# Performance work log

Measured on AMD Instinct MI355X. Metric: run time of the kernel, lower is better.

The kernel has to match this reference:

```python
import jax, jax.numpy as jnp
from jax import lax
import numpy as np

IN, HID, OUT = 28, 64, 10


def _lstm_layer(x_seq, W_ih, W_hh, b_ih, b_hh):
    # x_seq: [B, T, in]; PyTorch gate order: i, f, g, o (stacked along 4H)
    B = x_seq.shape[0]
    H = W_hh.shape[1]
    # Precompute input projection for all timesteps: [B, T, 4H]
    x_proj = jnp.einsum('bti,gi->btg', x_seq, W_ih) + b_ih + b_hh

    def step(carry, xt):
        h, c = carry
        gates = xt + h @ W_hh.T  # [B, 4H]
        i, f, g, o = jnp.split(gates, 4, axis=-1)
        i = jax.nn.sigmoid(i)
        f = jax.nn.sigmoid(f)
        g = jnp.tanh(g)
        o = jax.nn.sigmoid(o)
        c = f * c + i * g
        h = o * jnp.tanh(c)
        return (h, c), h

    h0 = jnp.zeros((B, H), x_seq.dtype)
    (_, _), hs = lax.scan(step, (h0, h0), jnp.swapaxes(x_proj, 0, 1))
    return jnp.swapaxes(hs, 0, 1)  # [B, T, H]


def setup_inputs() -> dict:
    key = jax.random.key(0)
    ks = jax.random.split(key, 12)
    s_in = 1.0 / np.sqrt(HID)
    u = lambda k, shape: jax.random.uniform(k, shape, jnp.float32, -s_in, s_in)
    return {
        'x': jax.random.normal(ks[0], (16384, 1, 28, 28), jnp.float32),
        'W_ih0': u(ks[1], (4 * HID, IN)),
        'W_hh0': u(ks[2], (4 * HID, HID)),
        'b_ih0': u(ks[3], (4 * HID,)),
        'b_hh0': u(ks[4], (4 * HID,)),
        'W_ih1': u(ks[5], (4 * HID, HID)),
        'W_hh1': u(ks[6], (4 * HID, HID)),
        'b_ih1': u(ks[7], (4 * HID,)),
        'b_hh1': u(ks[8], (4 * HID,)),
        'W_lin': u(ks[9], (OUT, HID)),
        'b_lin': u(ks[10], (OUT,)),
    }


def reference(x, W_ih0, W_hh0, b_ih0, b_hh0, W_ih1, W_hh1, b_ih1, b_hh1, W_lin, b_lin):
    # (N, C, H, W) -> (N, C*H, W): sequence of rows, feature = W = 28
    x = x.reshape(x.shape[0], -1, x.shape[-1])
    h1 = _lstm_layer(x, W_ih0, W_hh0, b_ih0, b_hh0)   # [B, T, 64]
    h2 = _lstm_layer(h1, W_ih1, W_hh1, b_ih1, b_hh1)  # [B, T, 64]
    last = h2[:, -1, :]
    return last @ W_lin.T + b_lin  # [B, 10]
```

## Files before the change

### kernel.cpp

```cpp
#include <hip/hip_runtime.h>


typedef _Float16 half8 __attribute__((ext_vector_type(8)));
typedef float floatx4 __attribute__((ext_vector_type(4)));

#define NFRAG 112
#define WS_BIAS_OFF (NFRAG * 1024)
#define K2 2.8853900817779268f

#if __has_builtin(__builtin_amdgcn_exp2f)
#define EXP2(v) __builtin_amdgcn_exp2f(v)
#else
#define EXP2(v) __expf(0.6931471805599453f * (v))
#endif
#define RCP(v) __builtin_amdgcn_rcpf(v)

__global__ void prep_kernel(const float* __restrict__ Wih0, const float* __restrict__ Whh0,
                            const float* __restrict__ bih0, const float* __restrict__ bhh0,
                            const float* __restrict__ Wih1, const float* __restrict__ Whh1,
                            const float* __restrict__ bih1, const float* __restrict__ bhh1,
                            _Float16* __restrict__ wA, float* __restrict__ wBias) {
    int idx = blockIdx.x * blockDim.x + threadIdx.x;
    if (idx < NFRAG * 512) {
        int f = idx >> 9, slot = idx & 511;
        int lane = slot >> 3, j = slot & 7;
        int mt, kt, layer;
        if (f < 48) { layer = 0; mt = f / 3; kt = f % 3; }
        else        { layer = 1; int f2 = f - 48; mt = f2 >> 2; kt = f2 & 3; }
        int m = mt * 16 + (lane & 15);
        int k = kt * 32 + (lane >> 4) * 8 + j;
        int u = m >> 2, g = m & 3;
        int row = g * 64 + u;
        float v;
        if (layer == 0) {
            if (k < 28)       v = Wih0[row * 28 + k];
            else if (k == 28) v = bih0[row] + bhh0[row];
            else if (k < 32)  v = 0.f;
            else              v = Whh0[row * 64 + (k - 32)];
        } else {
            if (k < 64)       v = Wih1[row * 64 + k];
            else              v = Whh1[row * 64 + (k - 64)];
        }
        float s = (g == 2) ? K2 : -1.4426950408889634f;
        wA[idx] = (_Float16)(v * s);
    } else if (idx < NFRAG * 512 + 256) {
        int m = idx - NFRAG * 512;
        int g = m & 3;
        int row = g * 64 + (m >> 2);
        float s = (g == 2) ? K2 : -1.4426950408889634f;
        wBias[m] = (bih1[row] + bhh1[row]) * s;
    }
}

template <int N>
__device__ __forceinline__ void gate_batch(const floatx4* acc, float* c,
                                           _Float16* const* planes, const int* offs) {
    float ei[N], ef[N], eg[N], eo[N];
    #pragma unroll
    for (int i = 0; i < N; ++i) {
        floatx4 a = acc[i];
        ei[i] = EXP2(a[0]);
        ef[i] = EXP2(a[1]);
        eg[i] = EXP2(a[2]);
        eo[i] = EXP2(a[3]);
    }
    float num[N], rd[N], po[N];
    #pragma unroll
    for (int i = 0; i < N; ++i) {
        float pi = 1.0f + ei[i];
        float pf = 1.0f + ef[i];
        float pg = 1.0f + eg[i];
        po[i] = 1.0f + eo[i];
        float m = pg * pi;
        num[i] = c[i] * m + (eg[i] - 1.0f) * pf;
        rd[i]  = RCP(pf * m);
    }
    float ec[N];
    #pragma unroll
    for (int i = 0; i < N; ++i) {
        float cn = num[i] * rd[i];
        c[i] = cn;
        ec[i] = EXP2(K2 * cn);
    }
    #pragma unroll
    for (int i = 0; i < N; ++i) {
        float r2 = RCP(ec[i] * po[i] + po[i]);
        planes[i][offs[i]] = (_Float16)((ec[i] - 1.0f) * r2);
    }
}

__launch_bounds__(512, 4)
__global__ void lstm_mfma(const float* __restrict__ x,
                          const _Float16* __restrict__ wA,
                          const float* __restrict__ wBias,
                          const float* __restrict__ Wlin, const float* __restrict__ blin,
                          float* __restrict__ out) {
    __shared__ __align__(16) _Float16 h0p[2][2048];
    __shared__ __align__(16) _Float16 h1p[2][2048];
    __shared__ __align__(16) _Float16 xb[2][1024];
    __shared__ float wlin_s[640];
    __shared__ float blin_s[10];

    const int lane = threadIdx.x;
    const int w    = threadIdx.y;
    const int tid  = w * 64 + lane;
    const int quad = lane >> 4;
    const int col  = lane & 15;
    const int l8   = lane * 8;
    const int nord = (w >> 2) & 1;

    half8 A0[2][3], A1[2][4];
    floatx4 bias1[2];
    int hwr0[2];
    #pragma unroll
    for (int j = 0; j < 2; ++j) {
        const int MT = 2 * w + j;
        #pragma unroll
        for (int kt = 0; kt < 3; ++kt)
            A0[j][kt] = *(const half8*)(wA + (MT * 3 + kt) * 512 + l8);
        #pragma unroll
        for (int kt = 0; kt < 4; ++kt)
            A1[j][kt] = *(const half8*)(wA + (48 + MT * 4 + kt) * 512 + l8);
        const int u = MT * 4 + quad;
        bias1[j] = *(const floatx4*)(wBias + u * 4);
        hwr0[j] = (u >> 5) * 512 + (((u >> 3) & 3) * 16 + col) * 8 + (u & 7);
    }

    const int ks = tid & 31;
    const bool xvalid = ks < 28;
    const int xbi = tid >> 5;
    const float* xg = x + (blockIdx.x * 32 + xbi) * 784 + ks;
    const int xstg = ((ks >> 3) * 16 + xbi) * 8 + (ks & 7);

    {
        ((int*)&h0p[1][0])[tid * 2 + 0] = 0;
        ((int*)&h0p[1][0])[tid * 2 + 1] = 0;
        ((int*)&h1p[1][0])[tid * 2 + 0] = 0;
        ((int*)&h1p[1][0])[tid * 2 + 1] = 0;
        float xv0 = xvalid ? xg[0] : 0.f;
        float xv1 = xvalid ? xg[16 * 784] : 0.f;
        _Float16 cpad = (ks == 28) ? (_Float16)1.0f : (_Float16)0.0f;
        xb[0][xstg]       = xvalid ? (_Float16)xv0 : cpad;
        xb[0][xstg + 512] = xvalid ? (_Float16)xv1 : cpad;
        xb[1][xstg]       = cpad;
        xb[1][xstg + 512] = cpad;
    }
    __syncthreads();

    float c0[2][2] = {{0.f, 0.f}, {0.f, 0.f}};
    float c1[2][2] = {{0.f, 0.f}, {0.f, 0.f}};

    for (int p = -1; p <= 27; ++p) {
        const int pr  = p & 1;
        const int pr1 = pr ^ 1;
        const bool doL0 = (p < 27);
        const bool doL1 = (p >= 0);

        float xn0 = 0.f, xn1 = 0.f;
        if (p <= 25 && xvalid) {
            xn0 = xg[(p + 2) * 28];
            xn1 = xg[16 * 784 + (p + 2) * 28];
        }

        #pragma unroll
        for (int pass = 0; pass < 2; ++pass) {
            const int in = nord ^ pass;
            const int hb = in << 10;

            half8 bx, bh0[2];
            if (doL0) bx = *(const half8*)&xb[pr1][(in << 9) + l8];
            #pragma unroll
            for (int kt = 0; kt < 2; ++kt)
                bh0[kt] = *(const half8*)&h0p[pr][hb + kt * 512 + l8];

            floatx4 acc0[2], acc1[2];
            if (doL0) {
                #pragma unroll
                for (int j = 0; j < 2; ++j) {
                    acc0[j] = __builtin_amdgcn_mfma_f32_16x16x32_f16(
                                  A0[j][0], bx, (floatx4){0.f, 0.f, 0.f, 0.f}, 0, 0, 0);
                    #pragma unroll
                    for (int kt = 0; kt < 2; ++kt)
                        acc0[j] = __builtin_amdgcn_mfma_f32_16x16x32_f16(
                                      A0[j][kt + 1], bh0[kt], acc0[j], 0, 0, 0);
                }
            }
            if (doL1) {
                #pragma unroll
                for (int j = 0; j < 2; ++j) {
                    acc1[j] = bias1[j];
                    #pragma unroll
                    for (int kt = 0; kt < 2; ++kt)
                        acc1[j] = __builtin_amdgcn_mfma_f32_16x16x32_f16(
                                      A1[j][kt], bh0[kt], acc1[j], 0, 0, 0);
                }
                half8 bh1[2];
                #pragma unroll
                for (int kt = 0; kt < 2; ++kt)
                    bh1[kt] = *(const half8*)&h1p[pr1][hb + kt * 512 + l8];
                #pragma unroll
                for (int j = 0; j < 2; ++j)
                    #pragma unroll
                    for (int kt = 0; kt < 2; ++kt)
                        acc1[j] = __builtin_amdgcn_mfma_f32_16x16x32_f16(
                                      A1[j][kt + 2], bh1[kt], acc1[j], 0, 0, 0);
            }

            const int offA = hwr0[0] + hb;
            const int offB = hwr0[1] + hb;
            if (doL0 && doL1) {
                floatx4 a4[4] = {acc0[0], acc0[1], acc1[0], acc1[1]};
                float   cc[4] = {c0[pass][0], c0[pass][1], c1[pass][0], c1[pass][1]};
                _Float16* pl[4] = {h0p[pr1], h0p[pr1], h1p[pr], h1p[pr]};
                int offs[4] = {offA, offB, offA, offB};
                gate_batch<4>(a4, cc, pl, offs);
                c0[pass][0] = cc[0]; c0[pass][1] = cc[1];
                c1[pass][0] = cc[2]; c1[pass][1] = cc[3];
            } else if (doL0) {
                floatx4 a2[2] = {acc0[0], acc0[1]};
                _Float16* pl[2] = {h0p[pr1], h0p[pr1]};
                int offs[2] = {offA, offB};
                gate_batch<2>(a2, c0[pass], pl, offs);
            } else {
                floatx4 a2[2] = {acc1[0], acc1[1]};
                _Float16* pl[2] = {h1p[pr], h1p[pr]};
                int offs[2] = {offA, offB};
                gate_batch<2>(a2, c1[pass], pl, offs);
            }
        }

        if (p <= 25 && xvalid) {
            xb[pr][xstg]       = (_Float16)xn0;
            xb[pr][xstg + 512] = (_Float16)xn1;
        }
        __syncthreads();
    }

    wlin_s[tid] = Wlin[tid];
    if (tid < 128) wlin_s[512 + tid] = Wlin[512 + tid];
    if (tid < 10)  blin_s[tid] = blin[tid];
    __syncthreads();
    if (tid < 320) {
        int b = tid / 10, o = tid - b * 10;
        float a = blin_s[o];
        #pragma unroll 8
        for (int uu = 0; uu < 64; ++uu) {
            float hv = (float)h1p[1][((b >> 4) * 2 + (uu >> 5)) * 512 + (((uu >> 3) & 3) * 16 + (b & 15)) * 8 + (uu & 7)];
            a += wlin_s[o * 64 + uu] * hv;
        }
        out[(blockIdx.x * 32 + b) * 10 + o] = a;
    }
}

extern "C" void kernel_launch(void* const* d_in, const int* in_sizes, int n_in,
                              void* d_out, int out_size, void* d_ws, size_t ws_size,
                              hipStream_t stream) {
    const float* x    = (const float*)d_in[0];
    const float* Wih0 = (const float*)d_in[1];
    const float* Whh0 = (const float*)d_in[2];
    const float* bih0 = (const float*)d_in[3];
    const float* bhh0 = (const float*)d_in[4];
    const float* Wih1 = (const float*)d_in[5];
    const float* Whh1 = (const float*)d_in[6];
    const float* bih1 = (const float*)d_in[7];
    const float* bhh1 = (const float*)d_in[8];
    const float* Wlin = (const float*)d_in[9];
    const float* blin = (const float*)d_in[10];
    float* out = (float*)d_out;

    _Float16* wA    = (_Float16*)d_ws;
    float*    wBias = (float*)((char*)d_ws + WS_BIAS_OFF);

    prep_kernel<<<225, 256, 0, stream>>>(Wih0, Whh0, bih0, bhh0,
                                         Wih1, Whh1, bih1, bhh1, wA, wBias);
    lstm_mfma<<<512, dim3(64, 8), 0, stream>>>(x, wA, wBias, Wlin, blin, out);
}
```

Measured before the change: 172.8 us.

## Merge two batch passes per step and peel loop into specialized phases

Each phase now processes both 16-column batch halves in one pass, issuing all MFMAs together and calling gate_batch on 8 accumulators at once, which exposes more independent MFMA and transcendental work per wavefront. The timestep loop is peeled into compile-time specialised phases, unrolled by two, so parity and layer-enable predicates become constants. Input staging switches to float2 loads of two adjacent elements per thread. The cost is higher register pressure from doubled live accumulators under the 512x4 launch bound, which could cause spills.

```diff
diff --git a/kernel.cpp b/kernel.cpp
--- a/kernel.cpp
+++ b/kernel.cpp
@@ -1,7 +1,8 @@
 #include <hip/hip_runtime.h>
 
 
-typedef _Float16 half8 __attribute__((ext_vector_type(8)));
+typedef _Float16 half8  __attribute__((ext_vector_type(8)));
+typedef _Float16 half2v __attribute__((ext_vector_type(2)));
 typedef float floatx4 __attribute__((ext_vector_type(4)));
 
 #define NFRAG 112
@@ -107,11 +108,10 @@
     const int quad = lane >> 4;
     const int col  = lane & 15;
     const int l8   = lane * 8;
-    const int nord = (w >> 2) & 1;
 
     half8 A0[2][3], A1[2][4];
     floatx4 bias1[2];
-    int hwr0[2];
+    int woff[2][2];
     #pragma unroll
     for (int j = 0; j < 2; ++j) {
         const int MT = 2 * w + j;
@@ -123,118 +123,147 @@
             A1[j][kt] = *(const half8*)(wA + (48 + MT * 4 + kt) * 512 + l8);
         const int u = MT * 4 + quad;
         bias1[j] = *(const floatx4*)(wBias + u * 4);
-        hwr0[j] = (u >> 5) * 512 + (((u >> 3) & 3) * 16 + col) * 8 + (u & 7);
-    }
-
-    const int ks = tid & 31;
-    const bool xvalid = ks < 28;
-    const int xbi = tid >> 5;
-    const float* xg = x + (blockIdx.x * 32 + xbi) * 784 + ks;
-    const int xstg = ((ks >> 3) * 16 + xbi) * 8 + (ks & 7);
+        const int hwr0 = (u >> 5) * 512 + (((u >> 3) & 3) * 16 + col) * 8 + (u & 7);
+        woff[j][0] = hwr0;
+        woff[j][1] = hwr0 + 1024;
+    }
+
+    const int scol = tid >> 4;
+    const int sm   = tid & 15;
+    const int k0   = 2 * sm;
+    const bool svalid = (sm < 14);
+    const int sin  = scol >> 4;
+    const int scl  = scol & 15;
+    const int xstg = (sin << 9) + ((k0 >> 3) * 16 + scl) * 8 + (k0 & 7);
+    const float* xptr = x + (blockIdx.x * 32 + scol) * 784 + k0;
 
     {
         ((int*)&h0p[1][0])[tid * 2 + 0] = 0;
         ((int*)&h0p[1][0])[tid * 2 + 1] = 0;
         ((int*)&h1p[1][0])[tid * 2 + 0] = 0;
         ((int*)&h1p[1][0])[tid * 2 + 1] = 0;
-        float xv0 = xvalid ? xg[0] : 0.f;
-        float xv1 = xvalid ? xg[16 * 784] : 0.f;
-        _Float16 cpad = (ks == 28) ? (_Float16)1.0f : (_Float16)0.0f;
-        xb[0][xstg]       = xvalid ? (_Float16)xv0 : cpad;
-        xb[0][xstg + 512] = xvalid ? (_Float16)xv1 : cpad;
-        xb[1][xstg]       = cpad;
-        xb[1][xstg + 512] = cpad;
+        if (!svalid) {
+            half2v cv;
+            cv[0] = (sm == 14) ? (_Float16)1.0f : (_Float16)0.0f;
+            cv[1] = (_Float16)0.0f;
+            *(half2v*)&xb[0][xstg] = cv;
+            *(half2v*)&xb[1][xstg] = cv;
+        } else {
+            float2 xv = *(const float2*)xptr;
+            half2v hv;
+            hv[0] = (_Float16)xv.x;
+            hv[1] = (_Float16)xv.y;
+            *(half2v*)&xb[0][xstg] = hv;
+        }
+        xptr += 28;
     }
     __syncthreads();
 
     float c0[2][2] = {{0.f, 0.f}, {0.f, 0.f}};
     float c1[2][2] = {{0.f, 0.f}, {0.f, 0.f}};
 
-    for (int p = -1; p <= 27; ++p) {
-        const int pr  = p & 1;
-        const int pr1 = pr ^ 1;
-        const bool doL0 = (p < 27);
-        const bool doL1 = (p >= 0);
-
-        float xn0 = 0.f, xn1 = 0.f;
-        if (p <= 25 && xvalid) {
-            xn0 = xg[(p + 2) * 28];
-            xn1 = xg[16 * 784 + (p + 2) * 28];
-        }
-
-        #pragma unroll
-        for (int pass = 0; pass < 2; ++pass) {
-            const int in = nord ^ pass;
-            const int hb = in << 10;
-
-            half8 bx, bh0[2];
-            if (doL0) bx = *(const half8*)&xb[pr1][(in << 9) + l8];
-            #pragma unroll
-            for (int kt = 0; kt < 2; ++kt)
-                bh0[kt] = *(const half8*)&h0p[pr][hb + kt * 512 + l8];
-
-            floatx4 acc0[2], acc1[2];
-            if (doL0) {
-                #pragma unroll
-                for (int j = 0; j < 2; ++j) {
-                    acc0[j] = __builtin_amdgcn_mfma_f32_16x16x32_f16(
-                                  A0[j][0], bx, (floatx4){0.f, 0.f, 0.f, 0.f}, 0, 0, 0);
-                    #pragma unroll
-                    for (int kt = 0; kt < 2; ++kt)
-                        acc0[j] = __builtin_amdgcn_mfma_f32_16x16x32_f16(
-                                      A0[j][kt + 1], bh0[kt], acc0[j], 0, 0, 0);
-                }
-            }
-            if (doL1) {
-                #pragma unroll
-                for (int j = 0; j < 2; ++j) {
-                    acc1[j] = bias1[j];
-                    #pragma unroll
-                    for (int kt = 0; kt < 2; ++kt)
-                        acc1[j] = __builtin_amdgcn_mfma_f32_16x16x32_f16(
-                                      A1[j][kt], bh0[kt], acc1[j], 0, 0, 0);
-                }
-                half8 bh1[2];
-                #pragma unroll
-                for (int kt = 0; kt < 2; ++kt)
-                    bh1[kt] = *(const half8*)&h1p[pr1][hb + kt * 512 + l8];
-                #pragma unroll
-                for (int j = 0; j < 2; ++j)
-                    #pragma unroll
-                    for (int kt = 0; kt < 2; ++kt)
-                        acc1[j] = __builtin_amdgcn_mfma_f32_16x16x32_f16(
-                                      A1[j][kt + 2], bh1[kt], acc1[j], 0, 0, 0);
-            }
-
-            const int offA = hwr0[0] + hb;
-            const int offB = hwr0[1] + hb;
-            if (doL0 && doL1) {
-                floatx4 a4[4] = {acc0[0], acc0[1], acc1[0], acc1[1]};
-                float   cc[4] = {c0[pass][0], c0[pass][1], c1[pass][0], c1[pass][1]};
-                _Float16* pl[4] = {h0p[pr1], h0p[pr1], h1p[pr], h1p[pr]};
-                int offs[4] = {offA, offB, offA, offB};
-                gate_batch<4>(a4, cc, pl, offs);
-                c0[pass][0] = cc[0]; c0[pass][1] = cc[1];
-                c1[pass][0] = cc[2]; c1[pass][1] = cc[3];
-            } else if (doL0) {
-                floatx4 a2[2] = {acc0[0], acc0[1]};
-                _Float16* pl[2] = {h0p[pr1], h0p[pr1]};
-                int offs[2] = {offA, offB};
-                gate_batch<2>(a2, c0[pass], pl, offs);
-            } else {
-                floatx4 a2[2] = {acc1[0], acc1[1]};
-                _Float16* pl[2] = {h1p[pr], h1p[pr]};
-                int offs[2] = {offA, offB};
-                gate_batch<2>(a2, c1[pass], pl, offs);
-            }
-        }
-
-        if (p <= 25 && xvalid) {
-            xb[pr][xstg]       = (_Float16)xn0;
-            xb[pr][xstg + 512] = (_Float16)xn1;
-        }
-        __syncthreads();
-    }
+#define PHASE(PR, DOL0, DOL1, DOSTAGE)                                              \
+    {                                                                               \
+        float2 xv2 = {0.f, 0.f};                                                    \
+        if ((DOSTAGE) && svalid) xv2 = *(const float2*)xptr;                        \
+        half8 bx[2], bh0[2][2];                                                     \
+        if (DOL0) {                                                                 \
+            bx[0] = *(const half8*)&xb[(PR) ^ 1][l8];                               \
+            bx[1] = *(const half8*)&xb[(PR) ^ 1][512 + l8];                         \
+        }                                                                           \
+        _Pragma("unroll")                                                           \
+        for (int kt = 0; kt < 2; ++kt) {                                            \
+            bh0[kt][0] = *(const half8*)&h0p[PR][kt * 512 + l8];                    \
+            bh0[kt][1] = *(const half8*)&h0p[PR][1024 + kt * 512 + l8];             \
+        }                                                                           \
+        floatx4 acc0[2][2], acc1[2][2];                                             \
+        if (DOL0) {                                                                 \
+            _Pragma("unroll")                                                       \
+            for (int j = 0; j < 2; ++j)                                             \
+                _Pragma("unroll")                                                   \
+                for (int in = 0; in < 2; ++in) {                                    \
+                    acc0[j][in] = __builtin_amdgcn_mfma_f32_16x16x32_f16(           \
+                        A0[j][0], bx[in], (floatx4){0.f, 0.f, 0.f, 0.f}, 0, 0, 0);  \
+                    _Pragma("unroll")                                               \
+                    for (int kt = 0; kt < 2; ++kt)                                  \
+                        acc0[j][in] = __builtin_amdgcn_mfma_f32_16x16x32_f16(       \
+                            A0[j][kt + 1], bh0[kt][in], acc0[j][in], 0, 0, 0);      \
+                }                                                                   \
+        }                                                                           \
+        if (DOL1) {                                                                 \
+            _Pragma("unroll")                                                       \
+            for (int j = 0; j < 2; ++j)                                             \
+                _Pragma("unroll")                                                   \
+                for (int in = 0; in < 2; ++in) {                                    \
+                    acc1[j][in] = bias1[j];                                         \
+                    _Pragma("unroll")                                               \
+                    for (int kt = 0; kt < 2; ++kt)                                  \
+                        acc1[j][in] = __builtin_amdgcn_mfma_f32_16x16x32_f16(       \
+                            A1[j][kt], bh0[kt][in], acc1[j][in], 0, 0, 0);          \
+                }                                                                   \
+            half8 bh1[2][2];                                                        \
+            _Pragma("unroll")                                                       \
+            for (int kt = 0; kt < 2; ++kt) {                                        \
+                bh1[kt][0] = *(const half8*)&h1p[(PR) ^ 1][kt * 512 + l8];          \
+                bh1[kt][1] = *(const half8*)&h1p[(PR) ^ 1][1024 + kt * 512 + l8];   \
+            }                                                                       \
+            _Pragma("unroll")                                                       \
+            for (int j = 0; j < 2; ++j)                                             \
+                _Pragma("unroll")                                                   \
+                for (int kt = 0; kt < 2; ++kt)                                      \
+                    _Pragma("unroll")                                               \
+                    for (int in = 0; in < 2; ++in)                                  \
+                        acc1[j][in] = __builtin_amdgcn_mfma_f32_16x16x32_f16(       \
+                            A1[j][kt + 2], bh1[kt][in], acc1[j][in], 0, 0, 0);      \
+        }                                                                           \
+        if ((DOL0) && (DOL1)) {                                                     \
+            floatx4 a8[8] = {acc0[0][0], acc0[0][1], acc0[1][0], acc0[1][1],        \
+                             acc1[0][0], acc1[0][1], acc1[1][0], acc1[1][1]};       \
+            float   cc[8] = {c0[0][0], c0[0][1], c0[1][0], c0[1][1],                \
+                             c1[0][0], c1[0][1], c1[1][0], c1[1][1]};               \
+            _Float16* pl[8] = {h0p[(PR) ^ 1], h0p[(PR) ^ 1], h0p[(PR) ^ 1],         \
+                               h0p[(PR) ^ 1], h1p[PR], h1p[PR], h1p[PR], h1p[PR]};  \
+            int offs[8] = {woff[0][0], woff[0][1], woff[1][0], woff[1][1],          \
+                           woff[0][0], woff[0][1], woff[1][0], woff[1][1]};         \
+            gate_batch<8>(a8, cc, pl, offs);                                        \
+            c0[0][0] = cc[0]; c0[0][1] = cc[1]; c0[1][0] = cc[2]; c0[1][1] = cc[3]; \
+            c1[0][0] = cc[4]; c1[0][1] = cc[5]; c1[1][0] = cc[6]; c1[1][1] = cc[7]; \
+        } else if (DOL0) {                                                          \
+            floatx4 a4[4] = {acc0[0][0], acc0[0][1], acc0[1][0], acc0[1][1]};       \
+            float   cc[4] = {c0[0][0], c0[0][1], c0[1][0], c0[1][1]};               \
+            _Float16* pl[4] = {h0p[(PR) ^ 1], h0p[(PR) ^ 1],                        \
+                               h0p[(PR) ^ 1], h0p[(PR) ^ 1]};                       \
+            int offs[4] = {woff[0][0], woff[0][1], woff[1][0], woff[1][1]};         \
+            gate_batch<4>(a4, cc, pl, offs);                                        \
+            c0[0][0] = cc[0]; c0[0][1] = cc[1]; c0[1][0] = cc[2]; c0[1][1] = cc[3]; \
+        } else {                                                                    \
+            floatx4 a4[4] = {acc1[0][0], acc1[0][1], acc1[1][0], acc1[1][1]};       \
+            float   cc[4] = {c1[0][0], c1[0][1], c1[1][0], c1[1][1]};               \
+            _Float16* pl[4] = {h1p[PR], h1p[PR], h1p[PR], h1p[PR]};                 \
+            int offs[4] = {woff[0][0], woff[0][1], woff[1][0], woff[1][1]};         \
+            gate_batch<4>(a4, cc, pl, offs);                                        \
+            c1[0][0] = cc[0]; c1[0][1] = cc[1]; c1[1][0] = cc[2]; c1[1][1] = cc[3]; \
+        }                                                                           \
+        if (DOSTAGE) {                                                              \
+            if (svalid) {                                                           \
+                half2v hv;                                                          \
+                hv[0] = (_Float16)xv2.x;                                            \
+                hv[1] = (_Float16)xv2.y;                                            \
+                *(half2v*)&xb[PR][xstg] = hv;                                       \
+            }                                                                       \
+            xptr += 28;                                                            \
+        }                                                                           \
+        __syncthreads();                                                            \
+    }
+
+    PHASE(1, true, false, true)
+    for (int i = 0; i < 13; ++i) {
+        PHASE(0, true, true, true)
+        PHASE(1, true, true, true)
+    }
+    PHASE(0, true, true, false)
+    PHASE(1, false, true, false)
+#undef PHASE
 
     wlin_s[tid] = Wlin[tid];
     if (tid < 128) wlin_s[512 + tid] = Wlin[512 + tid];
```

Measured after the change: 179.1 us. 3.7% more time.
